# Kernel tuning notes

Measured on AMD Instinct MI355X. Metric: run time of the kernel, lower is better.

The kernel has to match this reference:

```python
import jax, jax.numpy as jnp
import numpy as np

BN_EPS = 1e-4  # matches torch.nn.BatchNorm1d(eps=0.0001)

def setup_inputs() -> dict:
    key = jax.random.key(0)
    ks = jax.random.split(key, 8)
    N, T, D_in, D_out = 512, 64, 1024, 1024
    return {
        "input_feature_st": jax.random.randint(ks[0], (N, T, D_in), 0, 2).astype(jnp.float32),
        "input_features_sc": jax.random.normal(ks[1], (N, D_in), dtype=jnp.float32),
        "weight": jax.random.normal(ks[2], (D_out, D_in), dtype=jnp.float32) * 0.03,
        "bias": jax.random.normal(ks[3], (D_out,), dtype=jnp.float32) * 0.1,
        "gamma": jax.random.normal(ks[4], (D_out,), dtype=jnp.float32) * 2.0,  # nn.init.normal_(bn.weight, 0, 2.0)
        "beta": jnp.zeros((D_out,), dtype=jnp.float32),
        "running_mean": jax.random.normal(ks[5], (D_out,), dtype=jnp.float32) * 0.1,
        "running_var": jax.random.uniform(ks[6], (D_out,), dtype=jnp.float32, minval=0.5, maxval=1.5),
    }

def _if_scan(pot_in, bias_step):
    # pot_in: (N, T, D_out); bias_step: (D_out,) -> spikes (N, T, D_out)
    pot0 = jnp.zeros(pot_in.shape[::2], dtype=pot_in.dtype)  # (N, D_out)
    def step(pot, p_t):
        pot = pot + p_t + bias_step
        spk = (pot >= 1.0).astype(pot.dtype)
        return pot - spk, spk
    _, spikes_t = jax.lax.scan(step, pot0, jnp.swapaxes(pot_in, 0, 1))  # (T, N, D)
    return jnp.swapaxes(spikes_t, 0, 1)

def reference(input_feature_st, input_features_sc, weight, bias, gamma, beta, running_mean, running_var):
    T = input_feature_st.shape[1]
    # ANN path: Linear + BN (eval stats) + ReLU
    lin = input_features_sc @ weight.T + bias                      # (N, D_out)
    out_bn = gamma * (lin - running_mean) / jnp.sqrt(running_var + BN_EPS) + beta
    ann_output = jax.nn.relu(out_bn)
    # Fold BN into weights for the SNN path (note: no eps, as in source)
    ratio = gamma / jnp.sqrt(running_var)
    w_norm = weight * ratio[:, None]                               # (D_out, D_in)
    b_norm = (bias - running_mean) * ratio + beta                  # (D_out,)
    # Integrate-and-fire scan over T
    pot_in = jnp.einsum("ntd,od->nto", input_feature_st, w_norm)  # (N, T, D_out)
    spike_out = _if_scan(pot_in, b_norm / T)
    spike_count_out = jnp.sum(spike_out, axis=1)                   # (N, D_out)
    return spike_out, spike_count_out
```

## Files before the change

kernel.cpp:

```cpp
#include <hip/hip_runtime.h>
#include <hip/hip_bf16.h>

typedef float  float4v __attribute__((ext_vector_type(4)));
typedef short  short8v __attribute__((ext_vector_type(8)));
typedef short  short4v __attribute__((ext_vector_type(4)));
typedef __bf16 bf16x8  __attribute__((ext_vector_type(8)));
typedef float  f32x4   __attribute__((ext_vector_type(4)));

constexpr int NB = 512, T = 64, DIN = 1024, DOUT = 1024;
constexpr int BM = 128, BN = 128, BK = 64;
constexpr int LDA = 72;
constexpr int A_BYTES = BM * LDA * 2;
constexpr int B_BYTES = BN * BK * 2;
constexpr int SMEM_BYTES = A_BYTES + B_BYTES;

__device__ __forceinline__ short f2bf_rne(float x) {
    return __builtin_bit_cast(short, __float2bfloat16(x));
}
__device__ __forceinline__ short f2bf_trunc(float x) {
    return (short)(__builtin_bit_cast(unsigned int, x) >> 16);
}

__device__ __forceinline__ void load_lds_16B(const void* g, void* l) {
    __builtin_amdgcn_global_load_lds(
        (const __attribute__((address_space(1))) unsigned int*)g,
        (__attribute__((address_space(3))) unsigned int*)l, 16, 0, 0);
}

__global__ void __launch_bounds__(256)
fold_w_kernel(const float* __restrict__ W, const float* __restrict__ gamma,
              const float* __restrict__ rvar, __hip_bfloat16* __restrict__ Wn) {
    int idx = blockIdx.x * 256 + threadIdx.x;
    int o = idx >> 8;
    float r = gamma[o] / sqrtf(rvar[o]);
    float4v w = ((const float4v*)W)[idx];
    short4v s;
    #pragma unroll
    for (int j = 0; j < 4; j++) s[j] = f2bf_rne(w[j] * r);
    ((short4v*)Wn)[idx] = s;
}

template <bool PREFOLD>
__global__ void __launch_bounds__(256)
snn_gemm_if(const float* __restrict__ A,
            const float* __restrict__ W,
            const __hip_bfloat16* __restrict__ Wn,
            const float* __restrict__ bias, const float* __restrict__ gamma,
            const float* __restrict__ beta, const float* __restrict__ rmean,
            const float* __restrict__ rvar, float* __restrict__ out) {
    __shared__ __align__(16) char smem[SMEM_BYTES];
    __shared__ float ratioS[BN];
    __shared__ float bstepS[BN];
    short* AsS  = (short*)smem;
    short* BsS  = (short*)(smem + A_BYTES);
    float* potS = (float*)smem;

    const int tid   = threadIdx.x;
    const int by    = blockIdx.y;
    const int oBase = blockIdx.x * BN;

    if (tid < BN) {
        int o = oBase + tid;
        float r = gamma[o] / sqrtf(rvar[o]);
        ratioS[tid] = r;
        bstepS[tid] = ((bias[o] - rmean[o]) * r + beta[o]) * (1.0f / 64.0f);
    }
    __syncthreads();

    const int lane = tid & 63;
    const int wv   = tid >> 6;
    const int wr   = wv & 1;
    const int wc   = wv >> 1;
    const int l15  = lane & 15;
    const int quad = lane >> 4;

    f32x4 acc[4][4] = {};

    const float* Ab = A + (size_t)by * BM * DIN;

    for (int kb = 0; kb < DIN; kb += BK) {
        float4v av[4][2];
        #pragma unroll
        for (int i = 0; i < 4; i++) {
            int g = i * 256 + tid;
            int r = g >> 3, k8 = g & 7;
            const float4v* p = (const float4v*)(Ab + (size_t)r * DIN + kb + k8 * 8);
            av[i][0] = p[0];
            av[i][1] = p[1];
        }
        float4v bv[4][2];
        if constexpr (!PREFOLD) {
            #pragma unroll
            for (int i = 0; i < 4; i++) {
                int slot = i * 256 + tid;
                int r = slot >> 3, k8 = (slot & 7) ^ (r & 7);
                const float4v* p = (const float4v*)(W + (size_t)(oBase + r) * DIN + kb + k8 * 8);
                bv[i][0] = p[0];
                bv[i][1] = p[1];
            }
        }
        __syncthreads();

        if constexpr (PREFOLD) {
            #pragma unroll
            for (int i = 0; i < 4; i++) {
                int slot = i * 256 + tid;
                int r = slot >> 3, k8 = (slot & 7) ^ (r & 7);
                load_lds_16B(Wn + (size_t)(oBase + r) * DIN + kb + k8 * 8,
                             BsS + (size_t)slot * 8);
            }
        } else {
            #pragma unroll
            for (int i = 0; i < 4; i++) {
                int slot = i * 256 + tid;
                int r = slot >> 3;
                float rt = ratioS[r];
                short8v s;
                #pragma unroll
                for (int j = 0; j < 4; j++) {
                    s[j]     = f2bf_rne(bv[i][0][j] * rt);
                    s[j + 4] = f2bf_rne(bv[i][1][j] * rt);
                }
                *(short8v*)(BsS + (size_t)slot * 8) = s;
            }
        }
        #pragma unroll
        for (int i = 0; i < 4; i++) {
            int g = i * 256 + tid;
            int r = g >> 3, k8 = g & 7;
            short8v s;
            #pragma unroll
            for (int j = 0; j < 4; j++) {
                s[j]     = f2bf_trunc(av[i][0][j]);
                s[j + 4] = f2bf_trunc(av[i][1][j]);
            }
            *(short8v*)(&AsS[r * LDA + k8 * 8]) = s;
        }
        __syncthreads();

        #pragma unroll
        for (int ks = 0; ks < 2; ks++) {
            bf16x8 af[4], bfv[4];
            #pragma unroll
            for (int mi = 0; mi < 4; mi++)
                af[mi] = __builtin_bit_cast(bf16x8,
                    *(const short8v*)(&AsS[(wr * 64 + mi * 16 + l15) * LDA + ks * 32 + quad * 8]));
            #pragma unroll
            for (int ni = 0; ni < 4; ni++) {
                int row  = wc * 64 + ni * 16 + l15;
                int slot = row * 8 + ((ks * 4 + quad) ^ (l15 & 7));
                bfv[ni] = __builtin_bit_cast(bf16x8, *(const short8v*)(BsS + (size_t)slot * 8));
            }
            #pragma unroll
            for (int mi = 0; mi < 4; mi++)
                #pragma unroll
                for (int ni = 0; ni < 4; ni++)
                    acc[mi][ni] = __builtin_amdgcn_mfma_f32_16x16x32_bf16(
                        af[mi], bfv[ni], acc[mi][ni], 0, 0, 0);
        }
    }

    __syncthreads();

    #pragma unroll 1
    for (int s = 0; s < 2; s++) {
        if (wr == s) {
            #pragma unroll
            for (int mi = 0; mi < 4; mi++)
                #pragma unroll
                for (int ni = 0; ni < 4; ni++)
                    #pragma unroll
                    for (int r = 0; r < 4; r++)
                        potS[(mi * 16 + quad * 4 + r) * BN + wc * 64 + ni * 16 + l15] =
                            acc[mi][ni][r];
        }
        __syncthreads();
        if (tid < BN) {
            int n = by * 2 + s;
            float pot = 0.f, cnt = 0.f;
            const float bst = bstepS[tid];
            float* so = out + (size_t)n * T * DOUT + oBase + tid;
            for (int t = 0; t < T; t++) {
                pot += potS[t * BN + tid] + bst;
                float spk = (pot >= 1.0f) ? 1.0f : 0.0f;
                pot -= spk;
                cnt += spk;
                so[(size_t)t * DOUT] = spk;
            }
            out[(size_t)NB * T * DOUT + (size_t)n * DOUT + oBase + tid] = cnt;
        }
        __syncthreads();
    }
}

extern "C" void kernel_launch(void* const* d_in, const int* in_sizes, int n_in,
                              void* d_out, int out_size, void* d_ws, size_t ws_size,
                              hipStream_t stream) {
    const float* A     = (const float*)d_in[0];
    const float* W     = (const float*)d_in[2];
    const float* bias  = (const float*)d_in[3];
    const float* gamma = (const float*)d_in[4];
    const float* beta  = (const float*)d_in[5];
    const float* rmean = (const float*)d_in[6];
    const float* rvar  = (const float*)d_in[7];
    float* out = (float*)d_out;

    dim3 grid(DOUT / BN, NB / 2);
    const size_t wn_bytes = (size_t)DOUT * DIN * sizeof(__hip_bfloat16);
    if (d_ws != nullptr && ws_size >= wn_bytes) {
        __hip_bfloat16* Wn = (__hip_bfloat16*)d_ws;
        fold_w_kernel<<<DOUT * DIN / 4 / 256, 256, 0, stream>>>(W, gamma, rvar, Wn);
        snn_gemm_if<true><<<grid, 256, 0, stream>>>(A, W, Wn, bias, gamma, beta,
                                                    rmean, rvar, out);
    } else {
        snn_gemm_if<false><<<grid, 256, 0, stream>>>(A, W, nullptr, bias, gamma, beta,
                                                     rmean, rvar, out);
    }
}
```

Before: 368.3 us.

## Pre-convert activations to bf16 and stream both GEMM operands via LDS DMA

```diff
diff --git a/kernel.cpp b/kernel.cpp
--- a/kernel.cpp
+++ b/kernel.cpp
@@ -9,10 +9,10 @@
 
 constexpr int NB = 512, T = 64, DIN = 1024, DOUT = 1024;
 constexpr int BM = 128, BN = 128, BK = 64;
-constexpr int LDA = 72;
-constexpr int A_BYTES = BM * LDA * 2;
-constexpr int B_BYTES = BN * BK * 2;
-constexpr int SMEM_BYTES = A_BYTES + B_BYTES;
+
+constexpr size_t ABF_BYTES = (size_t)NB * T * DIN * 2;
+constexpr size_t WN_BYTES  = (size_t)DOUT * DIN * 2;
+constexpr size_t WS_BF16   = ABF_BYTES + WN_BYTES;
 
 __device__ __forceinline__ short f2bf_rne(float x) {
     return __builtin_bit_cast(short, __float2bfloat16(x));
@@ -20,7 +20,6 @@
 __device__ __forceinline__ short f2bf_trunc(float x) {
     return (short)(__builtin_bit_cast(unsigned int, x) >> 16);
 }
-
 __device__ __forceinline__ void load_lds_16B(const void* g, void* l) {
     __builtin_amdgcn_global_load_lds(
         (const __attribute__((address_space(1))) unsigned int*)g,
@@ -28,8 +27,23 @@
 }
 
 __global__ void __launch_bounds__(256)
+prep_a_kernel(const float* __restrict__ A, short* __restrict__ Abf) {
+    int idx = blockIdx.x * 256 + threadIdx.x;
+    const float4v* p = (const float4v*)A + (size_t)idx * 2;
+    float4v v0 = __builtin_nontemporal_load(p);
+    float4v v1 = __builtin_nontemporal_load(p + 1);
+    short8v s;
+    #pragma unroll
+    for (int j = 0; j < 4; j++) {
+        s[j]     = f2bf_trunc(v0[j]);
+        s[j + 4] = f2bf_trunc(v1[j]);
+    }
+    *((short8v*)Abf + idx) = s;
+}
+
+__global__ void __launch_bounds__(256)
 fold_w_kernel(const float* __restrict__ W, const float* __restrict__ gamma,
-              const float* __restrict__ rvar, __hip_bfloat16* __restrict__ Wn) {
+              const float* __restrict__ rvar, short* __restrict__ Wn) {
     int idx = blockIdx.x * 256 + threadIdx.x;
     int o = idx >> 8;
     float r = gamma[o] / sqrtf(rvar[o]);
@@ -40,32 +54,27 @@
     ((short4v*)Wn)[idx] = s;
 }
 
-template <bool PREFOLD>
-__global__ void __launch_bounds__(256)
-snn_gemm_if(const float* __restrict__ A,
-            const float* __restrict__ W,
-            const __hip_bfloat16* __restrict__ Wn,
-            const float* __restrict__ bias, const float* __restrict__ gamma,
-            const float* __restrict__ beta, const float* __restrict__ rmean,
-            const float* __restrict__ rvar, float* __restrict__ out) {
-    __shared__ __align__(16) char smem[SMEM_BYTES];
-    __shared__ float ratioS[BN];
+__global__ void __launch_bounds__(256, 4)
+snn_gemm_if_dma(const short* __restrict__ Abf,
+                const short* __restrict__ Wn,
+                const float* __restrict__ bias, const float* __restrict__ gamma,
+                const float* __restrict__ beta, const float* __restrict__ rmean,
+                const float* __restrict__ rvar, float* __restrict__ out) {
+    __shared__ __align__(16) char smem[32768];
     __shared__ float bstepS[BN];
-    short* AsS  = (short*)smem;
-    short* BsS  = (short*)(smem + A_BYTES);
+    char* AsS   = smem;
+    char* BsS   = smem + 16384;
     float* potS = (float*)smem;
 
-    const int tid   = threadIdx.x;
-    const int by    = blockIdx.y;
-    const int oBase = blockIdx.x * BN;
+    const int tid = threadIdx.x;
+    const int bs  = blockIdx.x;
+    const int oB  = blockIdx.y * BN;
 
     if (tid < BN) {
-        int o = oBase + tid;
+        int o = oB + tid;
         float r = gamma[o] / sqrtf(rvar[o]);
-        ratioS[tid] = r;
         bstepS[tid] = ((bias[o] - rmean[o]) * r + beta[o]) * (1.0f / 64.0f);
     }
-    __syncthreads();
 
     const int lane = tid & 63;
     const int wv   = tid >> 6;
@@ -74,8 +83,135 @@
     const int l15  = lane & 15;
     const int quad = lane >> 4;
 
+    int srcOff[4];
+    #pragma unroll
+    for (int i = 0; i < 4; i++) {
+        int s   = i * 256 + tid;
+        int row = s >> 3;
+        int ck  = (s & 7) ^ (row & 7);
+        srcOff[i] = (row * DIN + ck * 8) * 2;
+    }
+    int aOff[4][2], bOff[4][2];
+    #pragma unroll
+    for (int i = 0; i < 4; i++) {
+        int ra = wr * 64 + i * 16 + l15;
+        int rb = wc * 64 + i * 16 + l15;
+        #pragma unroll
+        for (int ks = 0; ks < 2; ks++) {
+            int c = ks * 4 + quad;
+            aOff[i][ks] = (ra * 8 + (c ^ (ra & 7))) * 16;
+            bOff[i][ks] = (rb * 8 + (c ^ (rb & 7))) * 16;
+        }
+    }
+
     f32x4 acc[4][4] = {};
-
+    const char* Ab = (const char*)(Abf + (size_t)bs * BM * DIN);
+    const char* Bb = (const char*)(Wn + (size_t)oB * DIN);
+
+    for (int kb = 0; kb < DIN; kb += BK) {
+        __syncthreads();
+        const int kbB = kb * 2;
+        #pragma unroll
+        for (int i = 0; i < 4; i++) {
+            int s = i * 256 + tid;
+            load_lds_16B(Ab + srcOff[i] + kbB, AsS + s * 16);
+            load_lds_16B(Bb + srcOff[i] + kbB, BsS + s * 16);
+        }
+        __syncthreads();
+
+        #pragma unroll
+        for (int ks = 0; ks < 2; ks++) {
+            bf16x8 af[4], bf[4];
+            #pragma unroll
+            for (int i = 0; i < 4; i++)
+                af[i] = __builtin_bit_cast(bf16x8, *(const short8v*)(AsS + aOff[i][ks]));
+            #pragma unroll
+            for (int i = 0; i < 4; i++)
+                bf[i] = __builtin_bit_cast(bf16x8, *(const short8v*)(BsS + bOff[i][ks]));
+            #pragma unroll
+            for (int mi = 0; mi < 4; mi++)
+                #pragma unroll
+                for (int ni = 0; ni < 4; ni++)
+                    acc[mi][ni] = __builtin_amdgcn_mfma_f32_16x16x32_bf16(
+                        af[mi], bf[ni], acc[mi][ni], 0, 0, 0);
+        }
+    }
+
+    __syncthreads();
+
+    #pragma unroll 1
+    for (int s = 0; s < 2; s++) {
+        if (wr == s) {
+            #pragma unroll
+            for (int mi = 0; mi < 4; mi++)
+                #pragma unroll
+                for (int ni = 0; ni < 4; ni++)
+                    #pragma unroll
+                    for (int r = 0; r < 4; r++) {
+                        int row = mi * 16 + quad * 4 + r;
+                        int col = (wc * 64 + ni * 16 + l15) ^ (quad << 3);
+                        potS[row * BN + col] = acc[mi][ni][r];
+                    }
+        }
+        __syncthreads();
+        if (tid < BN) {
+            int n = bs * 2 + s;
+            float pot = 0.f, cnt = 0.f;
+            const float bst = bstepS[tid];
+            float* so = out + (size_t)n * T * DOUT + oB + tid;
+            for (int t = 0; t < T; t++) {
+                pot += potS[t * BN + (tid ^ (((t >> 2) & 3) << 3))] + bst;
+                float spk = (pot >= 1.0f) ? 1.0f : 0.0f;
+                pot -= spk;
+                cnt += spk;
+                __builtin_nontemporal_store(spk, so + (size_t)t * DOUT);
+            }
+            __builtin_nontemporal_store(
+                cnt, out + (size_t)NB * T * DOUT + (size_t)n * DOUT + oB + tid);
+        }
+        __syncthreads();
+    }
+}
+
+
+constexpr int LDA_F = 72;
+constexpr int A_BYTES_F = BM * LDA_F * 2;
+constexpr int SMEM_F = A_BYTES_F + BN * BK * 2;
+
+template <bool PREFOLD>
+__global__ void __launch_bounds__(256)
+snn_gemm_if(const float* __restrict__ A, const float* __restrict__ W,
+            const short* __restrict__ Wn,
+            const float* __restrict__ bias, const float* __restrict__ gamma,
+            const float* __restrict__ beta, const float* __restrict__ rmean,
+            const float* __restrict__ rvar, float* __restrict__ out) {
+    __shared__ __align__(16) char smem[SMEM_F];
+    __shared__ float ratioS[BN];
+    __shared__ float bstepS[BN];
+    short* AsS  = (short*)smem;
+    short* BsS  = (short*)(smem + A_BYTES_F);
+    float* potS = (float*)smem;
+
+    const int tid   = threadIdx.x;
+    const int by    = blockIdx.y;
+    const int oBase = blockIdx.x * BN;
+
+    if (tid < BN) {
+        int o = oBase + tid;
+        float r = gamma[o] / sqrtf(rvar[o]);
+        ratioS[tid] = r;
+        bstepS[tid] = ((bias[o] - rmean[o]) * r + beta[o]) * (1.0f / 64.0f);
+    }
+    __syncthreads();
+
+    const int lane = tid & 63;
+    const int wv   = tid >> 6;
+    const int wr   = wv & 1;
+    const int wc   = wv >> 1;
+    const int l15  = lane & 15;
+    const int quad = lane >> 4;
+
+    f32x4 acc[4][4] = {};
     const float* Ab = A + (size_t)by * BM * DIN;
 
     for (int kb = 0; kb < DIN; kb += BK) {
@@ -134,7 +270,7 @@
                 s[j]     = f2bf_trunc(av[i][0][j]);
                 s[j + 4] = f2bf_trunc(av[i][1][j]);
             }
-            *(short8v*)(&AsS[r * LDA + k8 * 8]) = s;
+            *(short8v*)(&AsS[r * LDA_F + k8 * 8]) = s;
         }
         __syncthreads();
 
@@ -144,7 +280,7 @@
             #pragma unroll
             for (int mi = 0; mi < 4; mi++)
                 af[mi] = __builtin_bit_cast(bf16x8,
-                    *(const short8v*)(&AsS[(wr * 64 + mi * 16 + l15) * LDA + ks * 32 + quad * 8]));
+                    *(const short8v*)(&AsS[(wr * 64 + mi * 16 + l15) * LDA_F + ks * 32 + quad * 8]));
             #pragma unroll
             for (int ni = 0; ni < 4; ni++) {
                 int row  = wc * 64 + ni * 16 + l15;
@@ -205,14 +341,22 @@
     const float* rvar  = (const float*)d_in[7];
     float* out = (float*)d_out;
 
-    dim3 grid(DOUT / BN, NB / 2);
-    const size_t wn_bytes = (size_t)DOUT * DIN * sizeof(__hip_bfloat16);
-    if (d_ws != nullptr && ws_size >= wn_bytes) {
-        __hip_bfloat16* Wn = (__hip_bfloat16*)d_ws;
+    if (d_ws != nullptr && ws_size >= WS_BF16) {
+        short* Abf = (short*)d_ws;
+        short* Wn  = (short*)((char*)d_ws + ABF_BYTES);
+        prep_a_kernel<<<(NB * T * DIN) / 8 / 256, 256, 0, stream>>>(A, Abf);
         fold_w_kernel<<<DOUT * DIN / 4 / 256, 256, 0, stream>>>(W, gamma, rvar, Wn);
+        dim3 grid(NB / 2, DOUT / BN);
+        snn_gemm_if_dma<<<grid, 256, 0, stream>>>(Abf, Wn, bias, gamma, beta,
+                                                  rmean, rvar, out);
+    } else if (d_ws != nullptr && ws_size >= WN_BYTES) {
+        short* Wn = (short*)d_ws;
+        fold_w_kernel<<<DOUT * DIN / 4 / 256, 256, 0, stream>>>(W, gamma, rvar, Wn);
+        dim3 grid(DOUT / BN, NB / 2);
         snn_gemm_if<true><<<grid, 256, 0, stream>>>(A, W, Wn, bias, gamma, beta,
                                                     rmean, rvar, out);
     } else {
+        dim3 grid(DOUT / BN, NB / 2);
         snn_gemm_if<false><<<grid, 256, 0, stream>>>(A, W, nullptr, bias, gamma, beta,
                                                      rmean, rvar, out);
     }
```

Measured after the change: 306.2 us. 1.2x faster.
